# Kernel optimization log

Hardware: AMD Instinct MI355X
Metric: run time of the kernel (lower is better)

Reference implementation:

```python
import jax, jax.numpy as jnp
import numpy as np

V = 64                 # |Sigma|
IN_DIM = V + 2         # Sigma + '(' + ')'
OUT_DIM = V + 1        # Sigma + <del>/<end>
H = 512
B = 256
SX = 34                # max proto length 32 + 2 boundaries
SY = 34
BIG_NEG = -1000000000.0


def _one_hot_seq(key, S, batch):
    # '(' at pos 0, L random symbols, ')' at pos L+1, zero padding after
    kl, ks = jax.random.split(key)
    lengths = jax.random.randint(kl, (batch,), 4, S - 1)        # L in [4, S-2]
    syms = jax.random.randint(ks, (S, batch), 0, V)
    pos = jnp.arange(S)[:, None]
    tok = jnp.where(pos == 0, V, jnp.where(pos == lengths[None, :] + 1, V + 1, syms))
    oh = jax.nn.one_hot(tok, IN_DIM, dtype=jnp.float32)
    valid = (pos <= lengths[None, :] + 1).astype(jnp.float32)
    return oh * valid[:, :, None]


def setup_inputs() -> dict:
    key = jax.random.key(0)
    ks = jax.random.split(key, 14)

    def p(k, shape, scale):
        return jax.random.uniform(k, shape, jnp.float32, -scale, scale)

    s = 1.0 / float(np.sqrt(H))
    s2 = 1.0 / float(np.sqrt(2 * H))
    return {
        "sources": _one_hot_seq(ks[0], SX, B),
        "targets": _one_hot_seq(ks[1], SY, B),
        # bidirectional prior LSTM (input IN_DIM -> hidden H, fwd + rev)
        "Wih_f": p(ks[2], (4 * H, IN_DIM), s), "Whh_f": p(ks[3], (4 * H, H), s), "b_f": p(ks[4], (4 * H,), s),
        "Wih_r": p(ks[5], (4 * H, IN_DIM), s), "Whh_r": p(ks[6], (4 * H, H), s), "b_r": p(ks[7], (4 * H,), s),
        # modern LSTM (input IN_DIM -> hidden 2H)
        "Wih_m": p(ks[8], (8 * H, IN_DIM), s2), "Whh_m": p(ks[9], (8 * H, 2 * H), s2), "b_m": p(ks[10], (8 * H,), s2),
        # heads: Linear(2H -> OUT_DIM) + LogSoftmax
        "W_sub": p(ks[11], (OUT_DIM, 2 * H), s2), "b_sub": jnp.zeros((OUT_DIM,), jnp.float32),
        "W_ins": p(ks[12], (OUT_DIM, 2 * H), s2), "b_ins": jnp.zeros((OUT_DIM,), jnp.float32),
    }


def _lstm(x, Wih, Whh, b, hid):
    # torch gate order: i, f, g, o
    bsz = x.shape[1]
    def step(carry, xt):
        h, c = carry
        g = xt @ Wih.T + h @ Whh.T + b
        i, f, gg, o = jnp.split(g, 4, axis=-1)
        c = jax.nn.sigmoid(f) * c + jax.nn.sigmoid(i) * jnp.tanh(gg)
        h = jax.nn.sigmoid(o) * jnp.tanh(c)
        return (h, c), h
    init = (jnp.zeros((bsz, hid), x.dtype), jnp.zeros((bsz, hid), x.dtype))
    _, hs = jax.lax.scan(step, init, x)
    return hs  # [S, B, hid]


def _forward(sources, targets, Wih_f, Whh_f, b_f, Wih_r, Whh_r, b_r,
             Wih_m, Whh_m, b_m, W_sub, b_sub, W_ins, b_ins):
    x_fwd = _lstm(sources, Wih_f, Whh_f, b_f, H)
    x_bwd = _lstm(sources[::-1], Wih_r, Whh_r, b_r, H)[::-1]
    x_emb = jnp.concatenate([x_fwd, x_bwd], axis=-1)   # [SX, B, 2H]
    y_emb = _lstm(targets, Wih_m, Whh_m, b_m, 2 * H)    # [SY, B, 2H]

    # head(x_emb[i] + y_emb[j]) decomposes since Linear is affine
    def pair_logprobs(W, bb):
        lx = jnp.einsum('ibh,oh->ibo', x_emb, W)              # [SX, B, O]
        ly = jnp.einsum('jbh,oh->jbo', y_emb, W) + bb         # [SY, B, O]
        return jax.nn.log_softmax(lx[:, None] + ly[None, :], axis=-1)  # [SX, SY, B, O]

    sub_log = pair_logprobs(W_sub, b_sub)
    ins_log = pair_logprobs(W_ins, b_ins)

    # cell (i, j, b) is computed iff x[i] and y[j] are real (non-padding) one-hots, j <= max_cognat_length
    x_any = sources.sum(-1) > 0                                # [SX, B]
    y_any = targets.sum(-1) > 0                                # [SY, B]
    j_ok = jnp.arange(SY) < SY - 1
    valid = x_any[:, None, :] & (y_any & j_ok[:, None])[None, :, :]   # [SX, SY, B]

    end = jnp.where(valid, ins_log[..., V], BIG_NEG)           # insProbs[V_SIZE]
    dlt = jnp.where(valid, sub_log[..., V], BIG_NEG)           # subProbs[V_SIZE]

    y_next = jnp.pad(targets[1:], ((0, 1), (0, 0), (0, 0)))    # y[j+1], [SY, B, IN_DIM]
    ins_ok = valid & (y_next[..., IN_DIM - 1] == 0)[None]      # not bool(y[j+1, V_SIZE+1])
    ins_val = jnp.einsum('ijbv,jbv->ijb', ins_log[..., :V], y_next[..., :V])
    sub_val = jnp.einsum('ijbv,jbv->ijb', sub_log[..., :V], y_next[..., :V])

    # stacked cached probs: [ins, sub, end, del], each [SX, SY, B]
    return jnp.stack([
        jnp.where(ins_ok, ins_val, BIG_NEG),
        jnp.where(ins_ok, sub_val, BIG_NEG),
        end,
        dlt,
    ])


def reference(sources, targets, Wih_f, Whh_f, b_f, Wih_r, Whh_r, b_r,
              Wih_m, Whh_m, b_m, W_sub, b_sub, W_ins, b_ins):
    return _forward(sources, targets, Wih_f, Whh_f, b_f, Wih_r, Whh_r, b_r,
                    Wih_m, Whh_m, b_m, W_sub, b_sub, W_ins, b_ins)
```

## Files before the change

### kernel.cpp

```cpp
#include <hip/hip_runtime.h>

typedef __attribute__((ext_vector_type(4))) float f32x4;
typedef unsigned char u8;
typedef unsigned long long u64t;

#define BIG_NEG -1000000000.0f

static constexpr int B_  = 256;
static constexpr int SX_ = 34;
static constexpr int SY_ = 34;
static constexpr int IND = 66;
static constexpr int OP_ = 80;

__device__ __forceinline__ f32x4 mfma_fp8(long a, long b, f32x4 c) {
  return __builtin_amdgcn_mfma_f32_16x16x32_fp8_fp8(a, b, c, 0, 0, 0);
}
__device__ __forceinline__ float sigm(float x)  { return 1.0f / (1.0f + __expf(-x)); }
__device__ __forceinline__ float tanhx(float x) { return 2.0f * sigm(2.0f * x) - 1.0f; }
template <bool HI>
__device__ __forceinline__ unsigned pk2(float a, float b, unsigned old) {
  return __builtin_amdgcn_cvt_pk_fp8_f32(a, b, (int)old, HI);
}
__device__ __forceinline__ float rsel(f32x4 a, int j) {
  float lo = (j & 1) ? a[1] : a[0];
  float hi = (j & 1) ? a[3] : a[2];
  return (j & 2) ? hi : lo;
}

__global__ __launch_bounds__(256) void prep_all(
    const float* __restrict__ src, const float* __restrict__ tgt,
    int* __restrict__ tok_x, int* __restrict__ tok_y,
    const float* __restrict__ Wsub, const float* __restrict__ Wins,
    u8* __restrict__ Wcat,
    const float* __restrict__ Wihf, const float* __restrict__ bf,
    const float* __restrict__ Wihr, const float* __restrict__ br,
    const float* __restrict__ Wihm, const float* __restrict__ bm,
    float* __restrict__ Ef, float* __restrict__ Er, float* __restrict__ Em,
    const float* __restrict__ Whf, const float* __restrict__ Whr,
    const float* __restrict__ Whm,
    u8* __restrict__ w8f, u8* __restrict__ w8r, u8* __restrict__ w8m) {
  __shared__ float tile[64 * 67];
  const int blk = blockIdx.x;
  const int tid = threadIdx.x;

  if (blk < 68) {
    int idx = blk * 256 + tid;
    const int half = SX_ * B_;
    const float* base = (idx < half) ? src : tgt;
    int* outp         = (idx < half) ? tok_x : tok_y;
    int k = (idx < half) ? idx : idx - half;
    const float* p = base + (size_t)k * IND;
    int tok = -1;
    for (int v = 0; v < IND; ++v) if (p[v] > 0.5f) tok = v;
    outp[k] = tok;
  } else if (blk < 228) {
    int widx = (blk - 68) * 256 + tid;
    int row = widx >> 8;
    int wc  = widx & 255;
    int srow = row < 80 ? row : row - 80;
    const float* W = row < 80 ? Wsub : Wins;
    float f0 = 0.f, f1 = 0.f, f2 = 0.f, f3 = 0.f;
    if (srow < 65) {
      const float* p = W + (size_t)srow * 1024 + wc * 4;
      f0 = p[0]; f1 = p[1]; f2 = p[2]; f3 = p[3];
    }
    unsigned w = pk2<false>(f0, f1, 0);
    w = pk2<true>(f2, f3, w);
    ((unsigned*)Wcat)[widx] = w;
  } else if (blk < 356) {
    int tb = blk - 228;
    const float* W; const float* bias; float* E; int H4; int n0;
    if (tb < 32)      { W = Wihf; bias = bf; E = Ef; H4 = 2048; n0 = tb * 64; }
    else if (tb < 64) { W = Wihr; bias = br; E = Er; H4 = 2048; n0 = (tb - 32) * 64; }
    else              { W = Wihm; bias = bm; E = Em; H4 = 4096; n0 = (tb - 64) * 64; }
    const float* s2 = W + (size_t)n0 * IND;
    for (int i = tid; i < 64 * IND; i += 256) {
      int n = i / IND, v = i - n * IND;
      tile[n * 67 + v] = s2[i];
    }
    __syncthreads();
    int lane = tid & 63, w2 = tid >> 6;
    float bl = bias[n0 + lane];
    for (int v = w2; v < 67; v += 4) {
      float val = (v < 66 ? tile[lane * 67 + v] : 0.f) + bl;
      E[(size_t)v * H4 + n0 + lane] = val;
    }
  } else {
    const int F4 = 2048 * 512 / 4;
    const int M4 = 4096 * 1024 / 4;
    int i = (blk - 356) * 256 + tid;
    int stride = 3072 * 256;
    for (; i < 2 * F4 + M4; i += stride) {
      const float* s3; unsigned* dst; int k;
      if (i < F4)          { s3 = Whf; dst = (unsigned*)w8f; k = i; }
      else if (i < 2 * F4) { s3 = Whr; dst = (unsigned*)w8r; k = i - F4; }
      else                 { s3 = Whm; dst = (unsigned*)w8m; k = i - 2 * F4; }
      float4 f = ((const float4*)s3)[k];
      unsigned w3 = pk2<false>(f.x, f.y, 0);
      w3 = pk2<true>(f.z, f.w, w3);
      dst[k] = w3;
    }
  }
}


template <int HH, int NS>
__device__ __forceinline__ void run_lstm32(
    const u8* __restrict__ w8, const float* __restrict__ E,
    bool revr, u8* __restrict__ hall, int b0, int h0,
    unsigned* __restrict__ flags, int dom0, int myid,
    u8* __restrict__ alds, u8* __restrict__ hT, const u8* __restrict__ tok_small) {
  const int tid = threadIdx.x;
  const int lane = tid & 63, w = tid >> 6;
  const int lo = lane & 15, q = lane >> 4;
  constexpr int AST = HH + 8;
  constexpr int U8C = HH / 8;
  constexpr int USH = (HH == 1024) ? 7 : 6;
  constexpr int NI  = (32 * U8C) / 256;
  constexpr int NK  = HH / 32;
  const int hh = lo & 7;
  const bool hi = (lo >= 8);
  const int hu_e = h0 + w * 8 + hh;

  long breg0[NK], breg1[NK];
  {
    const u8* brow0 = w8 + (size_t)((lo >> 3) * HH + hu_e) * HH + q * 8;
    const u8* brow1 = w8 + (size_t)((2 + (lo >> 3)) * HH + hu_e) * HH + q * 8;
#pragma unroll
    for (int kk = 0; kk < NK; ++kk) {
      breg0[kk] = *(const long*)(brow0 + kk * 32);
      breg1[kk] = *(const long*)(brow1 + kk * 32);
    }
  }
  float creg[4] = {0.f, 0.f, 0.f, 0.f};

  for (int t = 0; t < 34; ++t) {
    const int tpos = revr ? 33 - t : t;
    const u8* tkp = tok_small + tpos * 32;

    float ev[2][4][2];
#pragma unroll
    for (int mt = 0; mt < 2; ++mt)
#pragma unroll
      for (int rr = 0; rr < 2; ++rr) {
        int r = (hi ? 2 : 0) + rr;
        int v = tkp[mt * 16 + q * 4 + r];
        const float* e = E + (size_t)v * (4 * HH) + hu_e;
        ev[mt][0][rr] = e[0];
        ev[mt][1][rr] = e[HH];
        ev[mt][2][rr] = e[2 * HH];
        ev[mt][3][rr] = e[3 * HH];
      }

    f32x4 acc[2][2];
#pragma unroll
    for (int mt = 0; mt < 2; ++mt) {
      acc[mt][0] = (f32x4){0.f, 0.f, 0.f, 0.f};
      acc[mt][1] = (f32x4){0.f, 0.f, 0.f, 0.f};
    }

    if (t > 0) {
      if (tid < NS) {
        const unsigned tgt = (unsigned)t;
        int spin = 0;
        for (;;) {
          unsigned v = __hip_atomic_load(&flags[(dom0 + tid) * 32],
                                         __ATOMIC_RELAXED, __HIP_MEMORY_SCOPE_AGENT);
          if (__ballot(v < tgt) == 0) break;
          __builtin_amdgcn_s_sleep(1);
          if (++spin > (1 << 17)) break;
        }
      }
      __syncthreads();

      const u8* hsrc = hall + (size_t)t * (256 * HH);
      u64t tmp[NI];
#pragma unroll
      for (int ii = 0; ii < NI; ++ii) {
        int idx = tid + ii * 256;
        tmp[ii] = __hip_atomic_load(
            (const u64t*)(hsrc + (size_t)(b0 + (idx >> USH)) * HH + (idx & (U8C - 1)) * 8),
            __ATOMIC_RELAXED, __HIP_MEMORY_SCOPE_AGENT);
      }
#pragma unroll
      for (int ii = 0; ii < NI; ++ii) {
        int idx = tid + ii * 256;
        *(u64t*)&alds[(idx >> USH) * AST + (idx & (U8C - 1)) * 8] = tmp[ii];
      }
      __syncthreads();

      const u8* a0p = alds + lo * AST + q * 8;
      const u8* a1p = alds + (16 + lo) * AST + q * 8;
#pragma unroll
      for (int kk = 0; kk < NK; ++kk) {
        long a0 = *(const long*)(a0p + kk * 32);
        long a1 = *(const long*)(a1p + kk * 32);
        acc[0][0] = mfma_fp8(a0, breg0[kk], acc[0][0]);
        acc[0][1] = mfma_fp8(a0, breg1[kk], acc[0][1]);
        acc[1][0] = mfma_fp8(a1, breg0[kk], acc[1][0]);
        acc[1][1] = mfma_fp8(a1, breg1[kk], acc[1][1]);
      }
    }

#pragma unroll
    for (int mt = 0; mt < 2; ++mt) {
      f32x4 t0 = acc[mt][0], t1 = acc[mt][1];
      f32x4 p0, p1;
#pragma unroll
      for (int c2 = 0; c2 < 4; ++c2) {
        p0[c2] = __shfl_xor(t0[c2], 8, 64);
        p1[c2] = __shfl_xor(t1[c2], 8, 64);
      }
#pragma unroll
      for (int rr = 0; rr < 2; ++rr) {
        int r = (hi ? 2 : 0) + rr;
        float iv = (hi ? p0[r] : t0[r]) + ev[mt][0][rr];
        float fv = (hi ? t0[r] : p0[r]) + ev[mt][1][rr];
        float gv = (hi ? p1[r] : t1[r]) + ev[mt][2][rr];
        float ov = (hi ? t1[r] : p1[r]) + ev[mt][3][rr];
        int m = mt * 16 + q * 4 + r;
        float cold = creg[mt * 2 + rr];
        float cn = sigm(fv) * cold + sigm(iv) * tanhx(gv);
        float hn = sigm(ov) * tanhx(cn);
        creg[mt * 2 + rr] = cn;
        hT[m * 32 + w * 8 + hh] = (u8)(pk2<false>(hn, hn, 0) & 0xffu);
      }
    }
    __syncthreads();

    {
      int m = tid >> 3, cc = tid & 7;
      unsigned val = *(const unsigned*)&hT[m * 32 + cc * 4];
      u8* hdst = hall + (size_t)(t + 1) * (256 * HH);
      __hip_atomic_store((unsigned*)(hdst + (size_t)(b0 + m) * HH + h0 + cc * 4),
                         val, __ATOMIC_RELAXED, __HIP_MEMORY_SCOPE_AGENT);
    }
    if (t < 33) {
      __asm__ volatile("s_waitcnt vmcnt(0)" ::: "memory");
      __syncthreads();
      if (tid == 0)
        __hip_atomic_store(&flags[(dom0 + myid) * 32], (unsigned)(t + 1),
                           __ATOMIC_RELAXED, __HIP_MEMORY_SCOPE_AGENT);
    }
  }
}

template <int HH, int NS>
__device__ __forceinline__ void run_lstm16(
    const u8* __restrict__ w8, const float* __restrict__ E,
    u8* __restrict__ hall, int b0, int h0,
    unsigned* __restrict__ flags, int dom0, int myid,
    u8* __restrict__ alds, u8* __restrict__ hT, const u8* __restrict__ tok_small) {
  const int tid = threadIdx.x;
  const int lane = tid & 63, w = tid >> 6;
  const int lo = lane & 15, q = lane >> 4;
  constexpr int AST = HH + 8;
  constexpr int U8C = HH / 8;
  constexpr int USH = 7;
  constexpr int NI  = (32 * U8C) / 256;
  constexpr int NK  = HH / 32;
  const int g = lo & 3;
  const int u = lo >> 2;
  const int hu = h0 + w * 4 + u;

  long breg[NK];
  {
    const u8* brow = w8 + (size_t)(g * HH + hu) * HH + q * 8;
#pragma unroll
    for (int kk = 0; kk < NK; ++kk) breg[kk] = *(const long*)(brow + kk * 32);
  }
  float creg[2] = {0.f, 0.f};

  for (int t = 0; t < 34; ++t) {
    const u8* tkp = tok_small + t * 32;

    float ev[2][4];
#pragma unroll
    for (int mt = 0; mt < 2; ++mt) {
      int v = tkp[mt * 16 + q * 4 + g];
      const float* e = E + (size_t)v * (4 * HH) + hu;
      ev[mt][0] = e[0]; ev[mt][1] = e[HH]; ev[mt][2] = e[2 * HH]; ev[mt][3] = e[3 * HH];
    }

    f32x4 acc[2];
    acc[0] = (f32x4){0.f, 0.f, 0.f, 0.f};
    acc[1] = (f32x4){0.f, 0.f, 0.f, 0.f};

    if (t > 0) {
      if (tid < NS) {
        const unsigned tgt = (unsigned)t;
        int spin = 0;
        for (;;) {
          unsigned v = __hip_atomic_load(&flags[(dom0 + tid) * 32],
                                         __ATOMIC_RELAXED, __HIP_MEMORY_SCOPE_AGENT);
          if (__ballot(v < tgt) == 0) break;
          __builtin_amdgcn_s_sleep(1);
          if (++spin > (1 << 17)) break;
        }
      }
      __syncthreads();

      const u8* hsrc = hall + (size_t)t * (256 * HH);
      u64t tmp[NI];
#pragma unroll
      for (int ii = 0; ii < NI; ++ii) {
        int idx = tid + ii * 256;
        tmp[ii] = __hip_atomic_load(
            (const u64t*)(hsrc + (size_t)(b0 + (idx >> USH)) * HH + (idx & (U8C - 1)) * 8),
            __ATOMIC_RELAXED, __HIP_MEMORY_SCOPE_AGENT);
      }
#pragma unroll
      for (int ii = 0; ii < NI; ++ii) {
        int idx = tid + ii * 256;
        *(u64t*)&alds[(idx >> USH) * AST + (idx & (U8C - 1)) * 8] = tmp[ii];
      }
      __syncthreads();

      const u8* a0p = alds + lo * AST + q * 8;
      const u8* a1p = alds + (16 + lo) * AST + q * 8;
#pragma unroll
      for (int kk = 0; kk < NK; ++kk) {
        long a0 = *(const long*)(a0p + kk * 32);
        long a1 = *(const long*)(a1p + kk * 32);
        acc[0] = mfma_fp8(a0, breg[kk], acc[0]);
        acc[1] = mfma_fp8(a1, breg[kk], acc[1]);
      }
    }

#pragma unroll
    for (int mt = 0; mt < 2; ++mt) {
      f32x4 a = acc[mt];
      float own = rsel(a, g);
      float y1  = __shfl_xor(rsel(a, g ^ 1), 1, 64);
      float y2  = __shfl_xor(rsel(a, g ^ 2), 2, 64);
      float y3  = __shfl_xor(rsel(a, g ^ 3), 3, 64);
      float iv = (g == 0) ? own : (g == 1) ? y1 : (g == 2) ? y2 : y3;
      float fv = (g == 0) ? y1 : (g == 1) ? own : (g == 2) ? y3 : y2;
      float gv = (g == 0) ? y2 : (g == 1) ? y3 : (g == 2) ? own : y1;
      float ov = (g == 0) ? y3 : (g == 1) ? y2 : (g == 2) ? y1 : own;
      iv += ev[mt][0]; fv += ev[mt][1]; gv += ev[mt][2]; ov += ev[mt][3];
      int m = mt * 16 + q * 4 + g;
      float cold = creg[mt];
      float cn = sigm(fv) * cold + sigm(iv) * tanhx(gv);
      float hn = sigm(ov) * tanhx(cn);
      creg[mt] = cn;
      hT[m * 16 + w * 4 + u] = (u8)(pk2<false>(hn, hn, 0) & 0xffu);
    }
    __syncthreads();

    if (tid < 128) {
      int m = tid >> 2, cc = tid & 3;
      unsigned val = *(const unsigned*)&hT[m * 16 + cc * 4];
      u8* hdst = hall + (size_t)(t + 1) * (256 * HH);
      __hip_atomic_store((unsigned*)(hdst + (size_t)(b0 + m) * HH + h0 + cc * 4),
                         val, __ATOMIC_RELAXED, __HIP_MEMORY_SCOPE_AGENT);
    }
    if (t < 33) {
      __asm__ volatile("s_waitcnt vmcnt(0)" ::: "memory");
      __syncthreads();
      if (tid == 0)
        __hip_atomic_store(&flags[(dom0 + myid) * 32], (unsigned)(t + 1),
                           __ATOMIC_RELAXED, __HIP_MEMORY_SCOPE_AGENT);
    }
  }
}

__global__ __launch_bounds__(256, 3) void lstm_persist(
    const int* __restrict__ tok_x, const int* __restrict__ tok_y,
    const float* __restrict__ E_f, const u8* __restrict__ w8_f,
    const float* __restrict__ E_r, const u8* __restrict__ w8_r,
    const float* __restrict__ E_m, const u8* __restrict__ w8_m,
    u8* __restrict__ fwd_all, u8* __restrict__ rev_all, u8* __restrict__ y_all,
    unsigned* __restrict__ flags) {
  __shared__ u8 alds[32 * 1032] __attribute__((aligned(16)));
  __shared__ u8 hT[32 * 32] __attribute__((aligned(16)));
  __shared__ u8 tok_small[34 * 32];

  const int b = blockIdx.x;
  int role, c, s;
  if (b < 512)      { role = 2; c = b >> 6; s = b & 63; }
  else if (b < 640) { int l = b - 512; role = 0; c = l >> 4; s = l & 15; }
  else              { int l = b - 640; role = 1; c = l >> 4; s = l & 15; }

  const float* E  = role == 0 ? E_f  : role == 1 ? E_r  : E_m;
  const u8*    w8 = role == 0 ? w8_f : role == 1 ? w8_r : w8_m;
  u8* hall        = role == 0 ? fwd_all : role == 1 ? rev_all : y_all;
  const int* tokg = (role == 2) ? tok_y : tok_x;
  const int b0 = c * 32;
  int dom0, h0;
  if (role == 2)      { dom0 = c * 64;       h0 = s * 16; }
  else if (role == 0) { dom0 = 512 + c * 16; h0 = s * 32; }
  else                { dom0 = 640 + c * 16; h0 = s * 32; }

  for (int i = threadIdx.x; i < 34 * 32; i += 256) {
    int t2 = i >> 5, m = i & 31;
    int tk = tokg[t2 * 256 + b0 + m];
    tok_small[i] = (u8)(tk < 0 ? 66 : tk);
  }
  __syncthreads();

  if (role == 2)
    run_lstm16<1024, 64>(w8, E, hall, b0, h0, flags, dom0, s, alds, hT, tok_small);
  else
    run_lstm32<512, 16>(w8, E, role == 1, hall, b0, h0, flags, dom0, s, alds, hT,
                        tok_small);
}

__global__ __launch_bounds__(256, 1) void head_kernel(
    const u8* __restrict__ fwd_all, const u8* __restrict__ rev_all,
    const u8* __restrict__ y_all, const u8* __restrict__ Wcat,
    const float* __restrict__ b_sub, const float* __restrict__ b_ins,
    float* __restrict__ lx_sub, float* __restrict__ lx_ins,
    float* __restrict__ ly_sub, float* __restrict__ ly_ins) {
  __shared__ u8 wq[160 * 264];
  const int lane = threadIdx.x & 63, wave = threadIdx.x >> 6;
  const int lo = lane & 15, q = lane >> 4;
  int blk = blockIdx.x;
  bool yside = (blk >= 136);
  int mb = yside ? blk - 136 : blk;
  int ij = mb >> 2;
  int bbase = (mb & 3) * 64;

  f32x4 acc[10];
#pragma unroll
  for (int nn = 0; nn < 10; ++nn) acc[nn] = (f32x4){0.f,0.f,0.f,0.f};

  for (int qk = 0; qk < 4; ++qk) {
    long aA[8];
    {
      int row = bbase + wave * 16 + lo;
      const u8* ab;
      if (yside)
        ab = y_all + ((size_t)(ij + 1) * 256 + row) * 1024 + qk * 256 + q * 8;
      else if (qk < 2)
        ab = fwd_all + ((size_t)(ij + 1) * 256 + row) * 512 + qk * 256 + q * 8;
      else
        ab = rev_all + ((size_t)(34 - ij) * 256 + row) * 512 + (qk - 2) * 256 + q * 8;
#pragma unroll
      for (int ki = 0; ki < 8; ++ki) aA[ki] = *(const long*)(ab + ki * 32);
    }

    for (int c8 = threadIdx.x; c8 < 160 * 32; c8 += 256) {
      int row = c8 >> 5, col = (c8 & 31) << 3;
      *(long*)&wq[row * 264 + col] =
          *(const long*)&Wcat[(size_t)row * 1024 + qk * 256 + col];
    }
    __syncthreads();

#pragma unroll
    for (int ki = 0; ki < 8; ++ki) {
#pragma unroll
      for (int nn = 0; nn < 10; ++nn) {
        long bf = *(const long*)&wq[(nn * 16 + lo) * 264 + ki * 32 + q * 8];
        acc[nn] = mfma_fp8(aA[ki], bf, acc[nn]);
      }
    }
    __syncthreads();
  }

#pragma unroll
  for (int nn = 0; nn < 10; ++nn) {
    bool is_sub = (nn < 5);
    int n = (is_sub ? nn : nn - 5) * 16 + lo;
    float bias = 0.0f;
    if (yside && n < 65) bias = is_sub ? b_sub[n] : b_ins[n];
    float* dst = yside ? (is_sub ? ly_sub : ly_ins) : (is_sub ? lx_sub : lx_ins);
#pragma unroll
    for (int r = 0; r < 4; ++r) {
      int b = bbase + wave * 16 + q * 4 + r;
      dst[((size_t)ij * 256 + b) * OP_ + n] = acc[nn][r] + bias;
    }
  }
}

__device__ __forceinline__ void lse_one(const float4* __restrict__ X,
                                        const float* __restrict__ py, int sym,
                                        float& logZ, float& v64, float& vs) {
  float v[68];
  const float4* py4 = (const float4*)py;
#pragma unroll
  for (int q = 0; q < 17; ++q) {
    float4 yb = py4[q];
    v[4 * q + 0] = X[q].x + yb.x;
    v[4 * q + 1] = X[q].y + yb.y;
    v[4 * q + 2] = X[q].z + yb.z;
    v[4 * q + 3] = X[q].w + yb.w;
  }
  float m = v[0];
#pragma unroll
  for (int o = 1; o < 65; ++o) m = fmaxf(m, v[o]);
  float s = 0.0f, vsl = 0.0f;
#pragma unroll
  for (int o = 0; o < 65; ++o) {
    s += __expf(v[o] - m);
    if (o < 64) vsl = (o == sym) ? v[o] : vsl;
  }
  logZ = m + __logf(s);
  v64 = v[64];
  vs = vsl;
}

__global__ __launch_bounds__(256, 1) void pair_kernel(
    const int* __restrict__ tok_x, const int* __restrict__ tok_y,
    const float* __restrict__ lx_sub, const float* __restrict__ lx_ins,
    const float* __restrict__ ly_sub, const float* __restrict__ ly_ins,
    float* __restrict__ out) {
  const int hsel = blockIdx.x >= 136;
  const int rem = hsel ? blockIdx.x - 136 : blockIdx.x;
  const int i = rem >> 2;
  const int bc = rem & 3;
  const int jq = threadIdx.x >> 6;
  const int bl = threadIdx.x & 63;
  const int b = bc * 64 + bl;
  const size_t CH = (size_t)SX_ * SY_ * B_;
  const float* lx = hsel ? lx_ins : lx_sub;
  const float* ly = hsel ? ly_ins : ly_sub;
  float* outA = out + (hsel ? 0 : CH);
  float* outB = out + (hsel ? 2 * CH : 3 * CH);

  float4 X[17];
  {
    const float4* ps = (const float4*)(lx + ((size_t)i * 256 + b) * OP_);
#pragma unroll
    for (int q = 0; q < 17; ++q) X[q] = ps[q];
  }
  int tx = tok_x[i * 256 + b];

  for (int j = jq; j < 34; j += 4) {
    size_t obase = ((size_t)i * SY_ + j) * 256 + b;
    bool dead = (j == SY_ - 1) || (tx < 0);
    if (!dead) {
      int ty = tok_y[j * 256 + b];
      if (ty < 0) dead = true;
    }
    if (dead) {
      outA[obase] = BIG_NEG;
      outB[obase] = BIG_NEG;
      continue;
    }
    int tn = tok_y[(j + 1) * 256 + b];
    bool ins_ok = (tn != 65);
    int sym = (tn >= 0 && tn < 64) ? tn : -1;

    float logZ, v64, vs;
    lse_one(X, ly + ((size_t)j * 256 + b) * OP_, sym, logZ, v64, vs);
    float valB = v64 - logZ;
    float valA = (sym >= 0) ? (vs - logZ) : 0.0f;
    outA[obase] = ins_ok ? valA : BIG_NEG;
    outB[obase] = valB;
  }
}

extern "C" void kernel_launch(void* const* d_in, const int* in_sizes, int n_in,
                              void* d_out, int out_size, void* d_ws, size_t ws_size,
                              hipStream_t stream) {
  const float* sources = (const float*)d_in[0];
  const float* targets = (const float*)d_in[1];
  const float* Wih_f = (const float*)d_in[2];
  const float* Whh_f = (const float*)d_in[3];
  const float* b_f   = (const float*)d_in[4];
  const float* Wih_r = (const float*)d_in[5];
  const float* Whh_r = (const float*)d_in[6];
  const float* b_r   = (const float*)d_in[7];
  const float* Wih_m = (const float*)d_in[8];
  const float* Whh_m = (const float*)d_in[9];
  const float* b_m   = (const float*)d_in[10];
  const float* W_sub = (const float*)d_in[11];
  const float* b_sub = (const float*)d_in[12];
  const float* W_ins = (const float*)d_in[13];
  const float* b_ins = (const float*)d_in[14];
  float* out = (float*)d_out;

  char* w = (char*)d_ws;
  constexpr size_t FLAG_SZ = 768 * 32 * 4;
  constexpr size_t TOK_SZ  = (size_t)SX_ * B_ * 4;
  constexpr size_t WCAT_SZ = (size_t)160 * 1024;
  constexpr size_t W8F_SZ  = (size_t)2048 * 512;
  constexpr size_t W8M_SZ  = (size_t)4096 * 1024;
  constexpr size_t EF_SZ   = (size_t)67 * 2048 * 4;
  constexpr size_t EM_SZ   = (size_t)67 * 4096 * 4;
  constexpr size_t LX_SZ   = (size_t)SX_ * B_ * OP_ * 4;
  constexpr size_t HF_SZ   = (size_t)35 * B_ * 512;
  constexpr size_t HM_SZ   = (size_t)35 * B_ * 1024;

  size_t off = 0;
  unsigned* flags = (unsigned*)(w + off); off += FLAG_SZ;
  int*  tok_x   = (int*)(w + off);  off += TOK_SZ;
  int*  tok_y   = (int*)(w + off);  off += TOK_SZ;
  off = (off + 255) & ~(size_t)255;
  u8*   Wcat    = (u8*)(w + off);   off += WCAT_SZ;
  u8*   w8_f    = (u8*)(w + off);   off += W8F_SZ;
  u8*   w8_r    = (u8*)(w + off);   off += W8F_SZ;
  u8*   w8_m    = (u8*)(w + off);   off += W8M_SZ;
  float* E_f    = (float*)(w + off); off += EF_SZ;
  float* E_r    = (float*)(w + off); off += EF_SZ;
  float* E_m    = (float*)(w + off); off += EM_SZ;
  float* lx_sub = (float*)(w + off); off += LX_SZ;
  float* lx_ins = (float*)(w + off); off += LX_SZ;
  float* ly_sub = (float*)(w + off); off += LX_SZ;
  float* ly_ins = (float*)(w + off); off += LX_SZ;
  u8* fwd_all   = (u8*)(w + off);   off += HF_SZ;
  u8* rev_all   = (u8*)(w + off);   off += HF_SZ;
  u8* y_all     = (u8*)(w + off);   off += HM_SZ;
  (void)ws_size; (void)in_sizes; (void)n_in; (void)out_size;

  (void)hipMemsetAsync(flags, 0, FLAG_SZ, stream);

  prep_all<<<3428, 256, 0, stream>>>(
      sources, targets, tok_x, tok_y,
      W_sub, W_ins, Wcat,
      Wih_f, b_f, Wih_r, b_r, Wih_m, b_m, E_f, E_r, E_m,
      Whh_f, Whh_r, Whh_m, w8_f, w8_r, w8_m);

  lstm_persist<<<768, 256, 0, stream>>>(
      tok_x, tok_y,
      E_f, w8_f,
      E_r, w8_r,
      E_m, w8_m,
      fwd_all, rev_all, y_all, flags);

  head_kernel<<<272, 256, 0, stream>>>(fwd_all, rev_all, y_all, Wcat,
                                       b_sub, b_ins, lx_sub, lx_ins, ly_sub, ly_ins);

  pair_kernel<<<272, 256, 0, stream>>>(tok_x, tok_y, lx_sub, lx_ins,
                                       ly_sub, ly_ins, out);
}
```

Measured before the change: 338.2 us.

## Fuse prep, LSTM, head and pair kernels into one persistent kernel with grid barriers

Merges the four launches into a single persistent 768-block kernel whose phases are separated by a global atomic-counter barrier. This removes three kernel-launch gaps and their tail effects. The pair phase's log-sum-exp is rewritten to stream the y-logits twice instead of holding a 68-float array, which lowers register pressure. The costs are that every block waits at each barrier even when only 272 blocks do head and pair work, and the barrier relies on all 768 blocks being co-resident (it also has a spin timeout).

Measured after the change: 601.2 us. +77.8%, slower.

```diff
diff --git a/kernel.cpp b/kernel.cpp
--- a/kernel.cpp
+++ b/kernel.cpp
@@ -11,6 +11,7 @@
 static constexpr int SY_ = 34;
 static constexpr int IND = 66;
 static constexpr int OP_ = 80;
+static constexpr int NBLK = 768;
 
 __device__ __forceinline__ f32x4 mfma_fp8(long a, long b, f32x4 c) {
   return __builtin_amdgcn_mfma_f32_16x16x32_fp8_fp8(a, b, c, 0, 0, 0);
@@ -27,82 +28,23 @@
   return (j & 2) ? hi : lo;
 }
 
-__global__ __launch_bounds__(256) void prep_all(
-    const float* __restrict__ src, const float* __restrict__ tgt,
-    int* __restrict__ tok_x, int* __restrict__ tok_y,
-    const float* __restrict__ Wsub, const float* __restrict__ Wins,
-    u8* __restrict__ Wcat,
-    const float* __restrict__ Wihf, const float* __restrict__ bf,
-    const float* __restrict__ Wihr, const float* __restrict__ br,
-    const float* __restrict__ Wihm, const float* __restrict__ bm,
-    float* __restrict__ Ef, float* __restrict__ Er, float* __restrict__ Em,
-    const float* __restrict__ Whf, const float* __restrict__ Whr,
-    const float* __restrict__ Whm,
-    u8* __restrict__ w8f, u8* __restrict__ w8r, u8* __restrict__ w8m) {
-  __shared__ float tile[64 * 67];
-  const int blk = blockIdx.x;
-  const int tid = threadIdx.x;
-
-  if (blk < 68) {
-    int idx = blk * 256 + tid;
-    const int half = SX_ * B_;
-    const float* base = (idx < half) ? src : tgt;
-    int* outp         = (idx < half) ? tok_x : tok_y;
-    int k = (idx < half) ? idx : idx - half;
-    const float* p = base + (size_t)k * IND;
-    int tok = -1;
-    for (int v = 0; v < IND; ++v) if (p[v] > 0.5f) tok = v;
-    outp[k] = tok;
-  } else if (blk < 228) {
-    int widx = (blk - 68) * 256 + tid;
-    int row = widx >> 8;
-    int wc  = widx & 255;
-    int srow = row < 80 ? row : row - 80;
-    const float* W = row < 80 ? Wsub : Wins;
-    float f0 = 0.f, f1 = 0.f, f2 = 0.f, f3 = 0.f;
-    if (srow < 65) {
-      const float* p = W + (size_t)srow * 1024 + wc * 4;
-      f0 = p[0]; f1 = p[1]; f2 = p[2]; f3 = p[3];
-    }
-    unsigned w = pk2<false>(f0, f1, 0);
-    w = pk2<true>(f2, f3, w);
-    ((unsigned*)Wcat)[widx] = w;
-  } else if (blk < 356) {
-    int tb = blk - 228;
-    const float* W; const float* bias; float* E; int H4; int n0;
-    if (tb < 32)      { W = Wihf; bias = bf; E = Ef; H4 = 2048; n0 = tb * 64; }
-    else if (tb < 64) { W = Wihr; bias = br; E = Er; H4 = 2048; n0 = (tb - 32) * 64; }
-    else              { W = Wihm; bias = bm; E = Em; H4 = 4096; n0 = (tb - 64) * 64; }
-    const float* s2 = W + (size_t)n0 * IND;
-    for (int i = tid; i < 64 * IND; i += 256) {
-      int n = i / IND, v = i - n * IND;
-      tile[n * 67 + v] = s2[i];
-    }
-    __syncthreads();
-    int lane = tid & 63, w2 = tid >> 6;
-    float bl = bias[n0 + lane];
-    for (int v = w2; v < 67; v += 4) {
-      float val = (v < 66 ? tile[lane * 67 + v] : 0.f) + bl;
-      E[(size_t)v * H4 + n0 + lane] = val;
-    }
-  } else {
-    const int F4 = 2048 * 512 / 4;
-    const int M4 = 4096 * 1024 / 4;
-    int i = (blk - 356) * 256 + tid;
-    int stride = 3072 * 256;
-    for (; i < 2 * F4 + M4; i += stride) {
-      const float* s3; unsigned* dst; int k;
-      if (i < F4)          { s3 = Whf; dst = (unsigned*)w8f; k = i; }
-      else if (i < 2 * F4) { s3 = Whr; dst = (unsigned*)w8r; k = i - F4; }
-      else                 { s3 = Whm; dst = (unsigned*)w8m; k = i - 2 * F4; }
-      float4 f = ((const float4*)s3)[k];
-      unsigned w3 = pk2<false>(f.x, f.y, 0);
-      w3 = pk2<true>(f.z, f.w, w3);
-      dst[k] = w3;
-    }
-  }
-}
-
+__device__ __forceinline__ void phase_barrier(unsigned* __restrict__ ctr) {
+  __asm__ volatile("s_waitcnt vmcnt(0)" ::: "memory");
+  __syncthreads();
+  if (threadIdx.x == 0) {
+    __hip_atomic_fetch_add(ctr, 1u, __ATOMIC_RELEASE, __HIP_MEMORY_SCOPE_AGENT);
+    int spin = 0;
+    for (;;) {
+      unsigned v = __hip_atomic_load(ctr, __ATOMIC_RELAXED, __HIP_MEMORY_SCOPE_AGENT);
+      if (v >= (unsigned)NBLK) break;
+      __builtin_amdgcn_s_sleep(2);
+      if (++spin > (1 << 20)) break;
+    }
+  }
+  __syncthreads();
+  __builtin_amdgcn_fence(__ATOMIC_ACQUIRE, "agent");
+  __syncthreads();
+}
 
 template <int HH, int NS>
 __device__ __forceinline__ void run_lstm32(
@@ -241,6 +183,9 @@
       if (tid == 0)
         __hip_atomic_store(&flags[(dom0 + myid) * 32], (unsigned)(t + 1),
                            __ATOMIC_RELAXED, __HIP_MEMORY_SCOPE_AGENT);
+    } else {
+      __asm__ volatile("s_waitcnt vmcnt(0)" ::: "memory");
+      __syncthreads();
     }
   }
 }
@@ -361,193 +306,266 @@
       if (tid == 0)
         __hip_atomic_store(&flags[(dom0 + myid) * 32], (unsigned)(t + 1),
                            __ATOMIC_RELAXED, __HIP_MEMORY_SCOPE_AGENT);
-    }
-  }
-}
-
-__global__ __launch_bounds__(256, 3) void lstm_persist(
-    const int* __restrict__ tok_x, const int* __restrict__ tok_y,
-    const float* __restrict__ E_f, const u8* __restrict__ w8_f,
-    const float* __restrict__ E_r, const u8* __restrict__ w8_r,
-    const float* __restrict__ E_m, const u8* __restrict__ w8_m,
-    u8* __restrict__ fwd_all, u8* __restrict__ rev_all, u8* __restrict__ y_all,
-    unsigned* __restrict__ flags) {
-  __shared__ u8 alds[32 * 1032] __attribute__((aligned(16)));
-  __shared__ u8 hT[32 * 32] __attribute__((aligned(16)));
-  __shared__ u8 tok_small[34 * 32];
-
-  const int b = blockIdx.x;
-  int role, c, s;
-  if (b < 512)      { role = 2; c = b >> 6; s = b & 63; }
-  else if (b < 640) { int l = b - 512; role = 0; c = l >> 4; s = l & 15; }
-  else              { int l = b - 640; role = 1; c = l >> 4; s = l & 15; }
-
-  const float* E  = role == 0 ? E_f  : role == 1 ? E_r  : E_m;
-  const u8*    w8 = role == 0 ? w8_f : role == 1 ? w8_r : w8_m;
-  u8* hall        = role == 0 ? fwd_all : role == 1 ? rev_all : y_all;
-  const int* tokg = (role == 2) ? tok_y : tok_x;
-  const int b0 = c * 32;
-  int dom0, h0;
-  if (role == 2)      { dom0 = c * 64;       h0 = s * 16; }
-  else if (role == 0) { dom0 = 512 + c * 16; h0 = s * 32; }
-  else                { dom0 = 640 + c * 16; h0 = s * 32; }
-
-  for (int i = threadIdx.x; i < 34 * 32; i += 256) {
-    int t2 = i >> 5, m = i & 31;
-    int tk = tokg[t2 * 256 + b0 + m];
-    tok_small[i] = (u8)(tk < 0 ? 66 : tk);
-  }
-  __syncthreads();
-
-  if (role == 2)
-    run_lstm16<1024, 64>(w8, E, hall, b0, h0, flags, dom0, s, alds, hT, tok_small);
-  else
-    run_lstm32<512, 16>(w8, E, role == 1, hall, b0, h0, flags, dom0, s, alds, hT,
-                        tok_small);
-}
-
-__global__ __launch_bounds__(256, 1) void head_kernel(
-    const u8* __restrict__ fwd_all, const u8* __restrict__ rev_all,
-    const u8* __restrict__ y_all, const u8* __restrict__ Wcat,
+    } else {
+      __asm__ volatile("s_waitcnt vmcnt(0)" ::: "memory");
+      __syncthreads();
+    }
+  }
+}
+
+__global__ __launch_bounds__(256, 3) void fused_all(
+    const float* __restrict__ src, const float* __restrict__ tgt,
+    int* __restrict__ tok_x, int* __restrict__ tok_y,
+    const float* __restrict__ Wsub, const float* __restrict__ Wins,
+    u8* __restrict__ Wcat,
+    const float* __restrict__ Wihf, const float* __restrict__ bf,
+    const float* __restrict__ Wihr, const float* __restrict__ br,
+    const float* __restrict__ Wihm, const float* __restrict__ bm,
+    float* __restrict__ Ef, float* __restrict__ Er, float* __restrict__ Em,
+    const float* __restrict__ Whf, const float* __restrict__ Whr,
+    const float* __restrict__ Whm,
+    u8* __restrict__ w8f, u8* __restrict__ w8r, u8* __restrict__ w8m,
     const float* __restrict__ b_sub, const float* __restrict__ b_ins,
     float* __restrict__ lx_sub, float* __restrict__ lx_ins,
-    float* __restrict__ ly_sub, float* __restrict__ ly_ins) {
-  __shared__ u8 wq[160 * 264];
-  const int lane = threadIdx.x & 63, wave = threadIdx.x >> 6;
-  const int lo = lane & 15, q = lane >> 4;
-  int blk = blockIdx.x;
-  bool yside = (blk >= 136);
-  int mb = yside ? blk - 136 : blk;
-  int ij = mb >> 2;
-  int bbase = (mb & 3) * 64;
-
-  f32x4 acc[10];
-#pragma unroll
-  for (int nn = 0; nn < 10; ++nn) acc[nn] = (f32x4){0.f,0.f,0.f,0.f};
-
-  for (int qk = 0; qk < 4; ++qk) {
-    long aA[8];
+    float* __restrict__ ly_sub, float* __restrict__ ly_ins,
+    u8* __restrict__ fwd_all, u8* __restrict__ rev_all, u8* __restrict__ y_all,
+    float* __restrict__ out, unsigned* __restrict__ flags) {
+  __shared__ u8 smem[160 * 264];
+  u8* alds = smem;
+  u8* hT   = smem + 33024;
+  u8* tok_small = smem + 34048;
+  float* tile = (float*)smem;
+  unsigned* bar = flags + 768 * 32;
+
+  const int blk = blockIdx.x;
+  const int tid = threadIdx.x;
+
+  for (int uu = blk; uu < 3428; uu += NBLK) {
+    if (uu < 68) {
+      int idx = uu * 256 + tid;
+      const int half = SX_ * B_;
+      const float* base = (idx < half) ? src : tgt;
+      int* outp         = (idx < half) ? tok_x : tok_y;
+      int k = (idx < half) ? idx : idx - half;
+      const float* p = base + (size_t)k * IND;
+      int tok = -1;
+      for (int v = 0; v < IND; ++v) if (p[v] > 0.5f) tok = v;
+      outp[k] = tok;
+    } else if (uu < 228) {
+      int widx = (uu - 68) * 256 + tid;
+      int row = widx >> 8;
+      int wc  = widx & 255;
+      int srow = row < 80 ? row : row - 80;
+      const float* W = row < 80 ? Wsub : Wins;
+      float f0 = 0.f, f1 = 0.f, f2 = 0.f, f3 = 0.f;
+      if (srow < 65) {
+        const float* p = W + (size_t)srow * 1024 + wc * 4;
+        f0 = p[0]; f1 = p[1]; f2 = p[2]; f3 = p[3];
+      }
+      unsigned wv = pk2<false>(f0, f1, 0);
+      wv = pk2<true>(f2, f3, wv);
+      ((unsigned*)Wcat)[widx] = wv;
+    } else if (uu < 356) {
+      int tb = uu - 228;
+      const float* W; const float* bias; float* E; int H4; int n0;
+      if (tb < 32)      { W = Wihf; bias = bf; E = Ef; H4 = 2048; n0 = tb * 64; }
+      else if (tb < 64) { W = Wihr; bias = br; E = Er; H4 = 2048; n0 = (tb - 32) * 64; }
+      else              { W = Wihm; bias = bm; E = Em; H4 = 4096; n0 = (tb - 64) * 64; }
+      const float* s2 = W + (size_t)n0 * IND;
+      __syncthreads();
+      for (int i = tid; i < 64 * IND; i += 256) {
+        int n = i / IND, v = i - n * IND;
+        tile[n * 67 + v] = s2[i];
+      }
+      __syncthreads();
+      int lane = tid & 63, w2 = tid >> 6;
+      float bl = bias[n0 + lane];
+      for (int v = w2; v < 67; v += 4) {
+        float val = (v < 66 ? tile[lane * 67 + v] : 0.f) + bl;
+        E[(size_t)v * H4 + n0 + lane] = val;
+      }
+    } else {
+      const int F4 = 2048 * 512 / 4;
+      const int M4 = 4096 * 1024 / 4;
+      int i = (uu - 356) * 256 + tid;
+      int stride = 3072 * 256;
+      for (; i < 2 * F4 + M4; i += stride) {
+        const float* s3; unsigned* dst; int k;
+        if (i < F4)          { s3 = Whf; dst = (unsigned*)w8f; k = i; }
+        else if (i < 2 * F4) { s3 = Whr; dst = (unsigned*)w8r; k = i - F4; }
+        else                 { s3 = Whm; dst = (unsigned*)w8m; k = i - 2 * F4; }
+        float4 f = ((const float4*)s3)[k];
+        unsigned w3 = pk2<false>(f.x, f.y, 0);
+        w3 = pk2<true>(f.z, f.w, w3);
+        dst[k] = w3;
+      }
+    }
+  }
+  phase_barrier(&bar[0]);
+
+  {
+    int role, c, s;
+    if (blk < 512)      { role = 2; c = blk >> 6; s = blk & 63; }
+    else if (blk < 640) { int l = blk - 512; role = 0; c = l >> 4; s = l & 15; }
+    else                { int l = blk - 640; role = 1; c = l >> 4; s = l & 15; }
+
+    const float* E  = role == 0 ? Ef  : role == 1 ? Er  : Em;
+    const u8*    w8 = role == 0 ? w8f : role == 1 ? w8r : w8m;
+    u8* hall        = role == 0 ? fwd_all : role == 1 ? rev_all : y_all;
+    const int* tokg = (role == 2) ? tok_y : tok_x;
+    const int b0 = c * 32;
+    int dom0, h0;
+    if (role == 2)      { dom0 = c * 64;       h0 = s * 16; }
+    else if (role == 0) { dom0 = 512 + c * 16; h0 = s * 32; }
+    else                { dom0 = 640 + c * 16; h0 = s * 32; }
+
+    for (int i = tid; i < 34 * 32; i += 256) {
+      int t2 = i >> 5, m = i & 31;
+      int tk = tokg[t2 * 256 + b0 + m];
+      tok_small[i] = (u8)(tk < 0 ? 66 : tk);
+    }
+    __syncthreads();
+
+    if (role == 2)
+      run_lstm16<1024, 64>(w8, E, hall, b0, h0, flags, dom0, s, alds, hT, tok_small);
+    else
+      run_lstm32<512, 16>(w8, E, role == 1, hall, b0, h0, flags, dom0, s, alds, hT,
+                          tok_small);
+  }
+  phase_barrier(&bar[32]);
+
+  if (blk < 272) {
+    u8* wq = smem;
+    const int lane = tid & 63, wave = tid >> 6;
+    const int lo = lane & 15, q = lane >> 4;
+    bool yside = (blk >= 136);
+    int mb = yside ? blk - 136 : blk;
+    int ij = mb >> 2;
+    int bbase = (mb & 3) * 64;
+
+    f32x4 acc[10];
+#pragma unroll
+    for (int nn = 0; nn < 10; ++nn) acc[nn] = (f32x4){0.f,0.f,0.f,0.f};
+
+    for (int qk = 0; qk < 4; ++qk) {
+      long aA[8];
+      {
+        int row = bbase + wave * 16 + lo;
+        const u8* ab;
+        if (yside)
+          ab = y_all + ((size_t)(ij + 1) * 256 + row) * 1024 + qk * 256 + q * 8;
+        else if (qk < 2)
+          ab = fwd_all + ((size_t)(ij + 1) * 256 + row) * 512 + qk * 256 + q * 8;
+        else
+          ab = rev_all + ((size_t)(34 - ij) * 256 + row) * 512 + (qk - 2) * 256 + q * 8;
+#pragma unroll
+        for (int ki = 0; ki < 8; ++ki) aA[ki] = *(const long*)(ab + ki * 32);
+      }
+
+      __syncthreads();
+      for (int c8 = tid; c8 < 160 * 32; c8 += 256) {
+        int row = c8 >> 5, col = (c8 & 31) << 3;
+        *(long*)&wq[row * 264 + col] =
+            *(const long*)&Wcat[(size_t)row * 1024 + qk * 256 + col];
+      }
+      __syncthreads();
+
+#pragma unroll
+      for (int ki = 0; ki < 8; ++ki) {
+#pragma unroll
+        for (int nn = 0; nn < 10; ++nn) {
+          long bfv = *(const long*)&wq[(nn * 16 + lo) * 264 + ki * 32 + q * 8];
+          acc[nn] = mfma_fp8(aA[ki], bfv, acc[nn]);
+        }
+      }
+    }
+
+#pragma unroll
+    for (int nn = 0; nn < 10; ++nn) {
+      bool is_sub = (nn < 5);
+      int n = (is_sub ? nn : nn - 5) * 16 + lo;
+      float bias = 0.0f;
+      if (yside && n < 65) bias = is_sub ? b_sub[n] : b_ins[n];
+      float* dst = yside ? (is_sub ? ly_sub : ly_ins) : (is_sub ? lx_sub : lx_ins);
+#pragma unroll
+      for (int r = 0; r < 4; ++r) {
+        int b = bbase + wave * 16 + q * 4 + r;
+        dst[((size_t)ij * 256 + b) * OP_ + n] = acc[nn][r] + bias;
+      }
+    }
+  }
+  phase_barrier(&bar[64]);
+
+  if (blk < 272) {
+    const int hsel = blk >= 136;
+    const int rem = hsel ? blk - 136 : blk;
+    const int i = rem >> 2;
+    const int bc = rem & 3;
+    const int jq = tid >> 6;
+    const int bl = tid & 63;
+    const int b = bc * 64 + bl;
+    const size_t CH = (size_t)SX_ * SY_ * B_;
+    const float* lx = hsel ? lx_ins : lx_sub;
+    const float* ly = hsel ? ly_ins : ly_sub;
+    float* outA = out + (hsel ? 0 : CH);
+    float* outB = out + (hsel ? 2 * CH : 3 * CH);
+
+    float4 X[17];
     {
-      int row = bbase + wave * 16 + lo;
-      const u8* ab;
-      if (yside)
-        ab = y_all + ((size_t)(ij + 1) * 256 + row) * 1024 + qk * 256 + q * 8;
-      else if (qk < 2)
-        ab = fwd_all + ((size_t)(ij + 1) * 256 + row) * 512 + qk * 256 + q * 8;
-      else
-        ab = rev_all + ((size_t)(34 - ij) * 256 + row) * 512 + (qk - 2) * 256 + q * 8;
-#pragma unroll
-      for (int ki = 0; ki < 8; ++ki) aA[ki] = *(const long*)(ab + ki * 32);
-    }
-
-    for (int c8 = threadIdx.x; c8 < 160 * 32; c8 += 256) {
-      int row = c8 >> 5, col = (c8 & 31) << 3;
-      *(long*)&wq[row * 264 + col] =
-          *(const long*)&Wcat[(size_t)row * 1024 + qk * 256 + col];
-    }
-    __syncthreads();
-
-#pragma unroll
-    for (int ki = 0; ki < 8; ++ki) {
-#pragma unroll
-      for (int nn = 0; nn < 10; ++nn) {
-        long bf = *(const long*)&wq[(nn * 16 + lo) * 264 + ki * 32 + q * 8];
-        acc[nn] = mfma_fp8(aA[ki], bf, acc[nn]);
-      }
-    }
-    __syncthreads();
-  }
-
-#pragma unroll
-  for (int nn = 0; nn < 10; ++nn) {
-    bool is_sub = (nn < 5);
-    int n = (is_sub ? nn : nn - 5) * 16 + lo;
-    float bias = 0.0f;
-    if (yside && n < 65) bias = is_sub ? b_sub[n] : b_ins[n];
-    float* dst = yside ? (is_sub ? ly_sub : ly_ins) : (is_sub ? lx_sub : lx_ins);
-#pragma unroll
-    for (int r = 0; r < 4; ++r) {
-      int b = bbase + wave * 16 + q * 4 + r;
-      dst[((size_t)ij * 256 + b) * OP_ + n] = acc[nn][r] + bias;
-    }
-  }
-}
-
-__device__ __forceinline__ void lse_one(const float4* __restrict__ X,
-                                        const float* __restrict__ py, int sym,
-                                        float& logZ, float& v64, float& vs) {
-  float v[68];
-  const float4* py4 = (const float4*)py;
-#pragma unroll
-  for (int q = 0; q < 17; ++q) {
-    float4 yb = py4[q];
-    v[4 * q + 0] = X[q].x + yb.x;
-    v[4 * q + 1] = X[q].y + yb.y;
-    v[4 * q + 2] = X[q].z + yb.z;
-    v[4 * q + 3] = X[q].w + yb.w;
-  }
-  float m = v[0];
-#pragma unroll
-  for (int o = 1; o < 65; ++o) m = fmaxf(m, v[o]);
-  float s = 0.0f, vsl = 0.0f;
-#pragma unroll
-  for (int o = 0; o < 65; ++o) {
-    s += __expf(v[o] - m);
-    if (o < 64) vsl = (o == sym) ? v[o] : vsl;
-  }
-  logZ = m + __logf(s);
-  v64 = v[64];
-  vs = vsl;
-}
-
-__global__ __launch_bounds__(256, 1) void pair_kernel(
-    const int* __restrict__ tok_x, const int* __restrict__ tok_y,
-    const float* __restrict__ lx_sub, const float* __restrict__ lx_ins,
-    const float* __restrict__ ly_sub, const float* __restrict__ ly_ins,
-    float* __restrict__ out) {
-  const int hsel = blockIdx.x >= 136;
-  const int rem = hsel ? blockIdx.x - 136 : blockIdx.x;
-  const int i = rem >> 2;
-  const int bc = rem & 3;
-  const int jq = threadIdx.x >> 6;
-  const int bl = threadIdx.x & 63;
-  const int b = bc * 64 + bl;
-  const size_t CH = (size_t)SX_ * SY_ * B_;
-  const float* lx = hsel ? lx_ins : lx_sub;
-  const float* ly = hsel ? ly_ins : ly_sub;
-  float* outA = out + (hsel ? 0 : CH);
-  float* outB = out + (hsel ? 2 * CH : 3 * CH);
-
-  float4 X[17];
-  {
-    const float4* ps = (const float4*)(lx + ((size_t)i * 256 + b) * OP_);
-#pragma unroll
-    for (int q = 0; q < 17; ++q) X[q] = ps[q];
-  }
-  int tx = tok_x[i * 256 + b];
-
-  for (int j = jq; j < 34; j += 4) {
-    size_t obase = ((size_t)i * SY_ + j) * 256 + b;
-    bool dead = (j == SY_ - 1) || (tx < 0);
-    if (!dead) {
-      int ty = tok_y[j * 256 + b];
-      if (ty < 0) dead = true;
-    }
-    if (dead) {
-      outA[obase] = BIG_NEG;
-      outB[obase] = BIG_NEG;
-      continue;
-    }
-    int tn = tok_y[(j + 1) * 256 + b];
-    bool ins_ok = (tn != 65);
-    int sym = (tn >= 0 && tn < 64) ? tn : -1;
-
-    float logZ, v64, vs;
-    lse_one(X, ly + ((size_t)j * 256 + b) * OP_, sym, logZ, v64, vs);
-    float valB = v64 - logZ;
-    float valA = (sym >= 0) ? (vs - logZ) : 0.0f;
-    outA[obase] = ins_ok ? valA : BIG_NEG;
-    outB[obase] = valB;
+      const float4* ps = (const float4*)(lx + ((size_t)i * 256 + b) * OP_);
+#pragma unroll
+      for (int qx = 0; qx < 17; ++qx) X[qx] = ps[qx];
+    }
+    int tx = tok_x[i * 256 + b];
+
+    for (int j = jq; j < 34; j += 4) {
+      size_t obase = ((size_t)i * SY_ + j) * 256 + b;
+      bool dead = (j == SY_ - 1) || (tx < 0);
+      if (!dead) {
+        int ty = tok_y[j * 256 + b];
+        if (ty < 0) dead = true;
+      }
+      if (dead) {
+        outA[obase] = BIG_NEG;
+        outB[obase] = BIG_NEG;
+        continue;
+      }
+      int tn = tok_y[(j + 1) * 256 + b];
+      bool ins_ok = (tn != 65);
+      int sym = (tn >= 0 && tn < 64) ? tn : -1;
+
+      const float4* py4 = (const float4*)(ly + ((size_t)j * 256 + b) * OP_);
+      float m = -3.0e38f;
+#pragma unroll
+      for (int qx = 0; qx < 16; ++qx) {
+        float4 yb = py4[qx];
+        float a0 = X[qx].x + yb.x, a1 = X[qx].y + yb.y;
+        float a2 = X[qx].z + yb.z, a3 = X[qx].w + yb.w;
+        m = fmaxf(m, fmaxf(fmaxf(a0, a1), fmaxf(a2, a3)));
+      }
+      float v64 = X[16].x + py4[16].x;
+      m = fmaxf(m, v64);
+      float s = 0.0f, vs = 0.0f;
+#pragma unroll
+      for (int qx = 0; qx < 16; ++qx) {
+        float4 yb = py4[qx];
+        float a0 = X[qx].x + yb.x, a1 = X[qx].y + yb.y;
+        float a2 = X[qx].z + yb.z, a3 = X[qx].w + yb.w;
+        s += __expf(a0 - m) + __expf(a1 - m) + __expf(a2 - m) + __expf(a3 - m);
+        int o0 = 4 * qx;
+        vs = (o0     == sym) ? a0 : vs;
+        vs = (o0 + 1 == sym) ? a1 : vs;
+        vs = (o0 + 2 == sym) ? a2 : vs;
+        vs = (o0 + 3 == sym) ? a3 : vs;
+      }
+      s += __expf(v64 - m);
+      float logZ = m + __logf(s);
+
+      float valB = v64 - logZ;
+      float valA = (sym >= 0) ? (vs - logZ) : 0.0f;
+      outA[obase] = ins_ok ? valA : BIG_NEG;
+      outB[obase] = valB;
+    }
   }
 }
 
@@ -572,7 +590,7 @@
   float* out = (float*)d_out;
 
   char* w = (char*)d_ws;
-  constexpr size_t FLAG_SZ = 768 * 32 * 4;
+  constexpr size_t FLAG_SZ = (size_t)(768 * 32 + 3 * 32) * 4;
   constexpr size_t TOK_SZ  = (size_t)SX_ * B_ * 4;
   constexpr size_t WCAT_SZ = (size_t)160 * 1024;
   constexpr size_t W8F_SZ  = (size_t)2048 * 512;
@@ -606,22 +624,11 @@
 
   (void)hipMemsetAsync(flags, 0, FLAG_SZ, stream);
 
-  prep_all<<<3428, 256, 0, stream>>>(
+  fused_all<<<NBLK, 256, 0, stream>>>(
       sources, targets, tok_x, tok_y,
       W_sub, W_ins, Wcat,
       Wih_f, b_f, Wih_r, b_r, Wih_m, b_m, E_f, E_r, E_m,
-      Whh_f, Whh_r, Whh_m, w8_f, w8_r, w8_m);
-
-  lstm_persist<<<768, 256, 0, stream>>>(
-      tok_x, tok_y,
-      E_f, w8_f,
-      E_r, w8_r,
-      E_m, w8_m,
-      fwd_all, rev_all, y_all, flags);
-
-  head_kernel<<<272, 256, 0, stream>>>(fwd_all, rev_all, y_all, Wcat,
-                                       b_sub, b_ins, lx_sub, lx_ins, ly_sub, ly_ins);
-
-  pair_kernel<<<272, 256, 0, stream>>>(tok_x, tok_y, lx_sub, lx_ins,
-                                       ly_sub, ly_ins, out);
-}
+      Whh_f, Whh_r, Whh_m, w8_f, w8_r, w8_m,
+      b_sub, b_ins, lx_sub, lx_ins, ly_sub, ly_ins,
+      fwd_all, rev_all, y_all, out, flags);
+}
```
